# Performance work log

Hardware: AMD Instinct MI355X
Metric: run time of the kernel (lower is better)

The kernel has to match this reference:

```python
import jax, jax.numpy as jnp
import numpy as np

PC_RANGE = (-54.0, -54.0, -5.0, 54.0, 54.0, 3.0)
VOXEL = (0.075, 0.075, 0.2)
STRIDE = 8
FW = 180  # feature map size along x
FH = 180  # feature map size along y
NUM_CLASS = 2
M = 500   # num_max_objs
MIN_RADIUS = 2
OVERLAP = 0.1
C_IN = 128
HM_C = 2
REG_C = 9
B = 4


def conv2d(x, w, b=None):
    y = jax.lax.conv_general_dilated(x, w, (1, 1), 'SAME',
                                     dimension_numbers=('NCHW', 'OIHW', 'NCHW'))
    return y if b is None else y + b[None, :, None, None]


def bn(x, g, b, m, v, eps=1e-5):
    inv = g / jnp.sqrt(v + eps)
    return x * inv[None, :, None, None] + (b - m * inv)[None, :, None, None]


def gaussian_radius(height, width, min_overlap):
    # centernet_utils.gaussian_radius
    b1 = height + width
    c1 = width * height * (1.0 - min_overlap) / (1.0 + min_overlap)
    r1 = (b1 + jnp.sqrt(jnp.maximum(b1 * b1 - 4.0 * c1, 0.0))) / 2.0
    b2 = 2.0 * (height + width)
    c2 = (1.0 - min_overlap) * width * height
    r2 = (b2 + jnp.sqrt(jnp.maximum(b2 * b2 - 16.0 * c2, 0.0))) / 2.0
    a3 = 4.0 * min_overlap
    b3 = -2.0 * min_overlap * (height + width)
    c3 = (min_overlap - 1.0) * width * height
    r3 = (b3 + jnp.sqrt(jnp.maximum(b3 * b3 - 4.0 * a3 * c3, 0.0))) / (2.0 * a3)
    return jnp.minimum(jnp.minimum(r1, r2), r3)


def assign_targets(gt):
    # gt: (B, M, 8) = [x, y, z, dx, dy, dz, ry, cls]; cls==0 / zero box = padding
    x, y, z = gt[..., 0], gt[..., 1], gt[..., 2]
    dx, dy, dz, ry = gt[..., 3], gt[..., 4], gt[..., 5], gt[..., 6]
    cls = gt[..., 7].astype(jnp.int32)
    coord_x = jnp.clip((x - PC_RANGE[0]) / VOXEL[0] / STRIDE, 0.0, FW - 0.5)
    coord_y = jnp.clip((y - PC_RANGE[1]) / VOXEL[1] / STRIDE, 0.0, FH - 0.5)
    cxi = coord_x.astype(jnp.int32)
    cyi = coord_y.astype(jnp.int32)
    dxp = dx / VOXEL[0] / STRIDE
    dyp = dy / VOXEL[1] / STRIDE
    radius = jnp.maximum(gaussian_radius(dxp, dyp, OVERLAP).astype(jnp.int32), MIN_RADIUS)
    valid = (dxp > 0) & (dyp > 0)
    pos = valid & (cls >= 1)

    # --- dense gaussian splat, max-reduced per class (= draw_gaussian_to_heatmap) ---
    ddx = jnp.arange(FW)[None, None, :] - cxi[..., None]   # (B,M,FW)
    ddy = jnp.arange(FH)[None, None, :] - cyi[..., None]   # (B,M,FH)
    sigma = (2.0 * radius.astype(jnp.float32) + 1.0) / 6.0
    d2 = (ddy[..., :, None] ** 2 + ddx[..., None, :] ** 2).astype(jnp.float32)  # (B,M,FH,FW)
    g = jnp.exp(-d2 / (2.0 * sigma[..., None, None] ** 2))
    win = (jnp.abs(ddy) <= radius[..., None])[..., :, None] & \
          (jnp.abs(ddx) <= radius[..., None])[..., None, :]
    g = jnp.where(win & pos[..., None, None], g, 0.0)
    seg = jnp.where(pos, cls - 1, NUM_CLASS)
    hmv = jax.vmap(lambda gv, sv: jax.ops.segment_max(gv, sv, num_segments=NUM_CLASS + 1))(
        g.reshape(B, M, FH * FW), seg)
    heatmap = jnp.maximum(hmv[:, :NUM_CLASS].reshape(B, NUM_CLASS, FH, FW), 0.0)
    heatmap_mask = (heatmap > 0).astype(gt.dtype)

    # --- inds / mask / ret_boxes (5 slots per object: center + 4 neighbors) ---
    base_ind = cyi * FW + cxi
    w_cond = VOXEL[0] * STRIDE > dy / 4.0   # faithful: uses temp_w = gt[:,4]
    l_cond = VOXEL[1] * STRIDE > dx / 4.0   # faithful: uses temp_l = gt[:,3]
    left = cxi - 1 >= 0
    right = cxi + 1 < FW
    up = cyi - 1 >= 0
    down = cyi + 1 < FH
    m0 = jnp.where(valid, jnp.where(cls >= 1, 1, -1), 0)
    s1 = valid & ~w_cond & left
    s2 = valid & ~w_cond & right
    s3 = valid & ~l_cond & up
    s4 = valid & ~l_cond & down
    mask = jnp.stack([m0,
                      jnp.where(s1, m0, 0), jnp.where(s2, m0, 0),
                      jnp.where(s3, m0, 0), jnp.where(s4, m0, 0)], -1).reshape(B, 5 * M)
    inds = jnp.stack([jnp.where(valid, base_ind, 0),
                      jnp.where(s1, base_ind - 1, 0), jnp.where(s2, base_ind + 1, 0),
                      jnp.where(s3, base_ind - FW, 0), jnp.where(s4, base_ind + FW, 0)],
                     -1).reshape(B, 5 * M).astype(jnp.int32)
    offx = coord_x - cxi.astype(gt.dtype)
    offy = coord_y - cyi.astype(gt.dtype)
    base = jnp.stack([offx, offy, z,
                      jnp.log(jnp.maximum(dx, 1e-8)),
                      jnp.log(jnp.maximum(dy, 1e-8)),
                      jnp.log(jnp.maximum(dz, 1e-8)),
                      jnp.cos(ry), jnp.sin(ry)], -1)          # (B,M,8)
    z5 = jnp.zeros((B, M), gt.dtype)
    dx_adj = jnp.stack([z5, s1.astype(gt.dtype), -s2.astype(gt.dtype), z5, z5], -1)  # (B,M,5)
    dy_adj = jnp.stack([z5, z5, z5, s3.astype(gt.dtype), -s4.astype(gt.dtype)], -1)
    zero5 = jnp.zeros_like(dx_adj)
    delta = jnp.stack([dx_adj, dy_adj, zero5, zero5, zero5, zero5, zero5, zero5], -1)  # (B,M,5,8)
    rb = (base[:, :, None, :] + delta) * valid[:, :, None, None].astype(gt.dtype)
    ret_boxes = rb.reshape(B, 5 * M, 8)
    return heatmap, ret_boxes, inds, mask, heatmap_mask


def setup_inputs():
    key = jax.random.key(0)
    ks = jax.random.split(key, 12)
    x = jax.random.normal(ks[0], (B, C_IN, FH, FW), jnp.float32)
    # realistic gt boxes; last 150 per scene are zero padding
    cxy = jax.random.uniform(ks[1], (B, M, 2), minval=-50.0, maxval=50.0)
    zc = jax.random.uniform(ks[2], (B, M, 1), minval=-2.0, maxval=1.0)
    dims = jax.random.uniform(ks[3], (B, M, 3), minval=0.5, maxval=6.0)
    ry = jax.random.uniform(ks[4], (B, M, 1), minval=-3.14, maxval=3.14)
    cls = jax.random.randint(ks[5], (B, M, 1), 1, NUM_CLASS + 1).astype(jnp.float32)
    vm = (jnp.arange(M) < 350)[None, :, None].astype(jnp.float32)
    gt_boxes = jnp.concatenate([cxy, zc, dims, ry, cls], -1) * vm
    p = lambda k, s, sc: jax.random.normal(k, s, jnp.float32) * sc
    return {
        'x': x, 'gt_boxes': gt_boxes,
        'conv1_w': p(ks[6], (C_IN, C_IN, 3, 3), 0.02),
        'bn1_g': jnp.ones((C_IN,)), 'bn1_b': jnp.zeros((C_IN,)),
        'bn1_m': jnp.zeros((C_IN,)), 'bn1_v': jnp.ones((C_IN,)),
        'conv2_w': p(ks[7], (C_IN, C_IN, 3, 3), 0.02),
        'bn2_g': jnp.ones((C_IN,)), 'bn2_b': jnp.zeros((C_IN,)),
        'bn2_m': jnp.zeros((C_IN,)), 'bn2_v': jnp.ones((C_IN,)),
        'hm_w': p(ks[8], (HM_C, C_IN, 3, 3), 0.02),
        'hm_b': jnp.full((HM_C,), -2.19, jnp.float32),
        'reg_w': p(ks[9], (REG_C, C_IN, 3, 3), 0.001),
        'reg_b': jnp.zeros((REG_C,), jnp.float32),
    }


def reference(x, gt_boxes, conv1_w, bn1_g, bn1_b, bn1_m, bn1_v,
              conv2_w, bn2_g, bn2_b, bn2_m, bn2_v, hm_w, hm_b, reg_w, reg_b):
    f = jax.nn.relu(bn(conv2d(x, conv1_w), bn1_g, bn1_b, bn1_m, bn1_v))
    f = jax.nn.relu(bn(conv2d(f, conv2_w), bn2_g, bn2_b, bn2_m, bn2_v))
    hm = conv2d(f, hm_w, hm_b)      # (B, 2, H, W)
    reg = conv2d(f, reg_w, reg_b)   # (B, 9, H, W)
    heatmap, ret_boxes, inds, mask, heatmap_mask = assign_targets(gt_boxes)
    return hm, reg, heatmap, ret_boxes, inds, mask, heatmap_mask
```

## Files before the change

### kernel.cpp

```cpp
#include <hip/hip_runtime.h>
#include <math.h>

typedef unsigned short u16;
typedef short bf16x8 __attribute__((ext_vector_type(8)));
typedef float f32x4 __attribute__((ext_vector_type(4)));

#define FW_ 180
#define FH_ 180
#define HW_ (FW_*FH_)
#define CIN_ 128
#define BB_ 4
#define MM_ 500
#define PW_ 182
#define PADE ((size_t)BB_*PW_*PW_*CIN_)

#define HM_OFF   0
#define REG_OFF  (BB_*2*HW_)
#define HEAT_OFF (REG_OFF + BB_*9*HW_)
#define RB_OFF   (HEAT_OFF + BB_*2*HW_)
#define IND_OFF  (RB_OFF + BB_*MM_*5*8)
#define MSK_OFF  (IND_OFF + BB_*MM_*5)
#define HMM_OFF  (MSK_OFF + BB_*MM_*5)

__device__ inline u16 f2bf(float f) {
    unsigned u = __float_as_uint(f);
    u += 0x7FFFu + ((u >> 16) & 1u);
    return (u16)(u >> 16);
}

#define GLOAD_LDS16(gsrc, ldst) \
    __builtin_amdgcn_global_load_lds( \
        (const __attribute__((address_space(1))) unsigned*)(gsrc), \
        (__attribute__((address_space(3))) unsigned*)(ldst), 16, 0, 0)

__global__ void k_init(u16* __restrict__ ws, float* __restrict__ out)
{
    int idx = blockIdx.x * 256 + threadIdx.x;
    const int n1 = 3 * BB_ * PW_ * PW_;
    if (idx < n1) {
        int buf = idx / (BB_ * PW_ * PW_);
        int rem = idx % (BB_ * PW_ * PW_);
        int p = rem % (PW_ * PW_);
        int r = p / PW_, c = p % PW_;
        if (r > 0 && r < PW_ - 1 && c > 0 && c < PW_ - 1) return;
        u16* base = ws + (size_t)buf * PADE + (size_t)rem * CIN_;
#pragma unroll
        for (int i = 0; i < 16; ++i) ((uint4*)base)[i] = make_uint4(0, 0, 0, 0);
    } else {
        int i = idx - n1;
        if (i < BB_ * 2 * HW_) out[HEAT_OFF + i] = 0.f;
    }
}

__global__ __launch_bounds__(256) void k_prep_xT(const float* __restrict__ in,
                                                 u16* __restrict__ xT)
{
    __shared__ unsigned lt32[180 * 65];
    int tid = threadIdx.x;
    int row = blockIdx.x, b = blockIdx.y;
    const float* inr = in + ((size_t)b * CIN_ * FH_ + row) * FW_;
    for (int i = tid; i < 64 * 45; i += 256) {
        int ci2 = i / 45, c4 = i - 45 * ci2;
        const float* p0 = inr + (size_t)(2 * ci2) * HW_ + c4 * 4;
        float4 a = *(const float4*)p0;
        float4 bq = *(const float4*)(p0 + HW_);
        lt32[(c4 * 4 + 0) * 65 + ci2] = (unsigned)f2bf(a.x) | ((unsigned)f2bf(bq.x) << 16);
        lt32[(c4 * 4 + 1) * 65 + ci2] = (unsigned)f2bf(a.y) | ((unsigned)f2bf(bq.y) << 16);
        lt32[(c4 * 4 + 2) * 65 + ci2] = (unsigned)f2bf(a.z) | ((unsigned)f2bf(bq.z) << 16);
        lt32[(c4 * 4 + 3) * 65 + ci2] = (unsigned)f2bf(a.w) | ((unsigned)f2bf(bq.w) << 16);
    }
    __syncthreads();
    unsigned* dst = (unsigned*)(xT + ((size_t)b * PW_ * PW_ + (size_t)(row + 1) * PW_ + 1) * CIN_);
    for (int idx = tid; idx < 180 * 64; idx += 256) {
        int col = idx >> 6, c2 = idx & 63;
        dst[col * 64 + c2] = lt32[col * 65 + c2];
    }
}

__global__ void k_prep_w(const float* __restrict__ w1, const float* __restrict__ w2,
                         const float* __restrict__ hw, const float* __restrict__ rw,
                         u16* __restrict__ wT1, u16* __restrict__ wT2,
                         u16* __restrict__ wTh)
{
    int i = blockIdx.x * 256 + threadIdx.x;
    const int NW = 9 * CIN_ * CIN_;
    if (i < NW) {
        int tap = i / (CIN_ * CIN_);
        int r = i % (CIN_ * CIN_);
        int co = r >> 7, ci = r & 127;
        wT1[i] = f2bf(w1[((size_t)co * CIN_ + ci) * 9 + tap]);
    } else if (i < 2 * NW) {
        int j = i - NW;
        int tap = j / (CIN_ * CIN_);
        int r = j % (CIN_ * CIN_);
        int co = r >> 7, ci = r & 127;
        wT2[j] = f2bf(w2[((size_t)co * CIN_ + ci) * 9 + tap]);
    } else {
        int j = i - 2 * NW;
        if (j >= 9 * 16 * CIN_) return;
        int tap = j / (16 * CIN_);
        int r = j % (16 * CIN_);
        int co = r >> 7, ci = r & 127;
        float v = 0.f;
        if (co < 2)       v = hw[((size_t)co * CIN_ + ci) * 9 + tap];
        else if (co < 11) v = rw[((size_t)(co - 2) * CIN_ + ci) * 9 + tap];
        wTh[j] = f2bf(v);
    }
}

__global__ __launch_bounds__(256) void k_conv_v5(
    const u16* __restrict__ xT, const u16* __restrict__ wT,
    const float* __restrict__ gg, const float* __restrict__ bbn,
    const float* __restrict__ mmn, const float* __restrict__ vvn,
    u16* __restrict__ yT)
{
    __shared__ u16 lin[1600 * 8];
    __shared__ u16 lwt[2304 * 8];

    int tid  = threadIdx.x;
    int wv   = tid >> 6, lane = tid & 63;
    int lm   = lane & 15, hi = lane >> 4;
    int csp  = blockIdx.x % 3, cog = blockIdx.x / 3;
    int C0   = (csp == 2) ? 116 : csp * 64;
    int cob  = cog * 64;
    int R0   = blockIdx.y * 4;
    int b    = blockIdx.z;
    const u16* xb = xT + (size_t)b * PW_ * PW_ * CIN_;

    f32x4 acc[4][4];
#pragma unroll
    for (int i = 0; i < 4; ++i)
#pragma unroll
        for (int j = 0; j < 4; ++j) acc[i][j] = (f32x4){0.f, 0.f, 0.f, 0.f};

    const int wco = (tid & 255) >> 2;
    const int wq  = (tid & 3) ^ ((wco >> 1) & 3);

#pragma unroll 1
    for (int ch = 0; ch < 4; ++ch) {
        int ci0 = ch * 32;
        __syncthreads();
#pragma unroll
        for (int rd = 0; rd < 6; ++rd) {
            int o = rd * 256 + tid;
            int rc = o >> 2;
            int r = rc / 66, c = rc - 66 * r;
            int q = (o & 3) ^ ((c >> 1) & 3);
            const u16* src = xb + ((size_t)(R0 + r) * PW_ + (C0 + c)) * CIN_ + ci0 + q * 8;
            GLOAD_LDS16(src, &lin[(size_t)(rd * 256 + wv * 64) * 8]);
        }
        if (wv == 0) {
            int o = 1536 + lane;
            int rc = o >> 2;
            int r = rc / 66, c = rc - 66 * r;
            if (o >= 1584) { r = 5; c = 65; }
            int q = (o & 3) ^ ((c >> 1) & 3);
            const u16* src = xb + ((size_t)(R0 + r) * PW_ + (C0 + c)) * CIN_ + ci0 + q * 8;
            GLOAD_LDS16(src, &lin[(size_t)1536 * 8]);
        }
#pragma unroll
        for (int tap = 0; tap < 9; ++tap) {
            const u16* src = wT + (size_t)tap * CIN_ * CIN_ + (size_t)(cob + wco) * CIN_ + ci0 + wq * 8;
            GLOAD_LDS16(src, &lwt[(size_t)(tap * 256 + wv * 64) * 8]);
        }
        __syncthreads();

#pragma unroll
        for (int tap = 0; tap < 9; ++tap) {
            const int kr = tap / 3, kc = tap - 3 * (tap / 3);
            bf16x8 av[4];
#pragma unroll
            for (int mf = 0; mf < 4; ++mf) {
                int col = mf * 16 + lm;
                int unit = tap * 256 + col * 4 + (hi ^ ((col >> 1) & 3));
                av[mf] = *(const bf16x8*)&lwt[(size_t)unit * 8];
            }
#pragma unroll
            for (int nf = 0; nf < 4; ++nf) {
                int c = wv * 16 + lm + kc;
                int rc = (nf + kr) * 66 + c;
                int unit = rc * 4 + (hi ^ ((c >> 1) & 3));
                bf16x8 bv = *(const bf16x8*)&lin[(size_t)unit * 8];
#pragma unroll
                for (int mf = 0; mf < 4; ++mf)
                    acc[mf][nf] = __builtin_amdgcn_mfma_f32_16x16x32_bf16(
                        av[mf], bv, acc[mf][nf], 0, 0, 0);
            }
        }
    }

#pragma unroll
    for (int mf = 0; mf < 4; ++mf) {
        int co0 = cob + mf * 16 + hi * 4;
        float4 g4 = *(const float4*)(gg + co0);
        float4 b4 = *(const float4*)(bbn + co0);
        float4 m4 = *(const float4*)(mmn + co0);
        float4 v4 = *(const float4*)(vvn + co0);
        float sc0 = g4.x / sqrtf(v4.x + 1e-5f), sh0 = b4.x - m4.x * sc0;
        float sc1 = g4.y / sqrtf(v4.y + 1e-5f), sh1 = b4.y - m4.y * sc1;
        float sc2 = g4.z / sqrtf(v4.z + 1e-5f), sh2 = b4.z - m4.z * sc2;
        float sc3 = g4.w / sqrtf(v4.w + 1e-5f), sh3 = b4.w - m4.w * sc3;
#pragma unroll
        for (int nf = 0; nf < 4; ++nf) {
            f32x4 A = acc[mf][nf];
            float y0 = fmaxf(fmaf(A[0], sc0, sh0), 0.f);
            float y1 = fmaxf(fmaf(A[1], sc1, sh1), 0.f);
            float y2 = fmaxf(fmaf(A[2], sc2, sh2), 0.f);
            float y3 = fmaxf(fmaf(A[3], sc3, sh3), 0.f);
            unsigned p0 = (unsigned)f2bf(y0) | ((unsigned)f2bf(y1) << 16);
            unsigned p1 = (unsigned)f2bf(y2) | ((unsigned)f2bf(y3) << 16);
            u16* op = yT + (size_t)b * PW_ * PW_ * CIN_ +
                      ((size_t)(R0 + nf + 1) * PW_ + (C0 + wv * 16 + lm + 1)) * CIN_ + co0;
            *(uint2*)op = make_uint2(p0, p1);
        }
    }
}

__global__ __launch_bounds__(256) void k_head_v5(
    const u16* __restrict__ f2T, const u16* __restrict__ wTh,
    const float* __restrict__ hb, const float* __restrict__ rb,
    float* __restrict__ out)
{
    __shared__ u16 lin[1600 * 8];
    __shared__ u16 lwt[2304 * 8];

    int tid  = threadIdx.x;
    int wv   = tid >> 6, lane = tid & 63;
    int lm   = lane & 15, hi = lane >> 4;
    int csp  = blockIdx.x;
    int C0   = (csp == 2) ? 116 : csp * 64;
    int R0   = blockIdx.y * 4;
    int b    = blockIdx.z;
    const u16* xb = f2T + (size_t)b * PW_ * PW_ * CIN_;

    f32x4 acc[4];
#pragma unroll
    for (int i = 0; i < 4; ++i) acc[i] = (f32x4){0.f, 0.f, 0.f, 0.f};

#pragma unroll
    for (int rd = 0; rd < 9; ++rd) {
        int o = rd * 256 + tid;
        int tap = o >> 8, rest = o & 255;
        int co = rest >> 4, u8s = rest & 15;
        const u16* src = wTh + (size_t)tap * 16 * CIN_ + co * CIN_ + ((u8s ^ (co & 7)) * 8);
        GLOAD_LDS16(src, &lwt[(size_t)(rd * 256 + wv * 64) * 8]);
    }

#pragma unroll 1
    for (int ch = 0; ch < 4; ++ch) {
        int ci0 = ch * 32;
        __syncthreads();
#pragma unroll
        for (int rd = 0; rd < 6; ++rd) {
            int o = rd * 256 + tid;
            int rc = o >> 2;
            int r = rc / 66, c = rc - 66 * r;
            int q = (o & 3) ^ ((c >> 1) & 3);
            const u16* src = xb + ((size_t)(R0 + r) * PW_ + (C0 + c)) * CIN_ + ci0 + q * 8;
            GLOAD_LDS16(src, &lin[(size_t)(rd * 256 + wv * 64) * 8]);
        }
        if (wv == 0) {
            int o = 1536 + lane;
            int rc = o >> 2;
            int r = rc / 66, c = rc - 66 * r;
            if (o >= 1584) { r = 5; c = 65; }
            int q = (o & 3) ^ ((c >> 1) & 3);
            const u16* src = xb + ((size_t)(R0 + r) * PW_ + (C0 + c)) * CIN_ + ci0 + q * 8;
            GLOAD_LDS16(src, &lin[(size_t)1536 * 8]);
        }
        __syncthreads();

#pragma unroll
        for (int tap = 0; tap < 9; ++tap) {
            const int kr = tap / 3, kc = tap - 3 * (tap / 3);
            int u8 = (ch * 4 + hi) ^ (lm & 7);
            bf16x8 av = *(const bf16x8*)&lwt[(size_t)(tap * 256 + lm * 16 + u8) * 8];
#pragma unroll
            for (int nf = 0; nf < 4; ++nf) {
                int c = wv * 16 + lm + kc;
                int rc = (nf + kr) * 66 + c;
                int unit = rc * 4 + (hi ^ ((c >> 1) & 3));
                bf16x8 bv = *(const bf16x8*)&lin[(size_t)unit * 8];
                acc[nf] = __builtin_amdgcn_mfma_f32_16x16x32_bf16(av, bv, acc[nf], 0, 0, 0);
            }
        }
    }

#pragma unroll
    for (int nf = 0; nf < 4; ++nf) {
        int row = R0 + nf, col = C0 + wv * 16 + lm;
        f32x4 A = acc[nf];
#pragma unroll
        for (int r = 0; r < 4; ++r) {
            int co = hi * 4 + r;
            float v = A[r];
            if (co < 2)
                out[HM_OFF + ((size_t)(b * 2 + co)) * HW_ + (size_t)row * FW_ + col] = v + hb[co];
            else if (co < 11)
                out[REG_OFF + ((size_t)(b * 9 + co - 2)) * HW_ + (size_t)row * FW_ + col] = v + rb[co - 2];
        }
    }
}

__global__ void k_objects(const float* __restrict__ gt, float* __restrict__ out)
{
    int ob = blockIdx.x;
    int b = ob / MM_, m = ob % MM_;
    const float* gp = gt + (size_t)ob * 8;
    float x = gp[0], y = gp[1], z = gp[2];
    float dx = gp[3], dy = gp[4], dz = gp[5], ry = gp[6];
    int cls = (int)gp[7];

    float coord_x = fminf(fmaxf((x + 54.f) / 0.075f / 8.f, 0.f), 179.5f);
    float coord_y = fminf(fmaxf((y + 54.f) / 0.075f / 8.f, 0.f), 179.5f);
    int cxi = (int)coord_x, cyi = (int)coord_y;
    float dxp = dx / 0.075f / 8.f;
    float dyp = dy / 0.075f / 8.f;

    float hgt = dxp, wid = dyp, mo = 0.1f;
    float b1 = hgt + wid, c1 = wid * hgt * (1.f - mo) / (1.f + mo);
    float r1 = (b1 + sqrtf(fmaxf(b1 * b1 - 4.f * c1, 0.f))) * 0.5f;
    float b2 = 2.f * (hgt + wid), c2 = (1.f - mo) * wid * hgt;
    float r2 = (b2 + sqrtf(fmaxf(b2 * b2 - 16.f * c2, 0.f))) * 0.5f;
    float a3 = 4.f * mo, b3 = -2.f * mo * (hgt + wid), c3 = (mo - 1.f) * wid * hgt;
    float r3 = (b3 + sqrtf(fmaxf(b3 * b3 - 4.f * a3 * c3, 0.f))) / (2.f * a3);
    int radius = max((int)fminf(fminf(r1, r2), r3), 2);

    bool valid = (dxp > 0.f) && (dyp > 0.f);
    bool pos = valid && (cls >= 1);

    if (threadIdx.x == 0) {
        float m0 = valid ? (cls >= 1 ? 1.f : -1.f) : 0.f;
        bool w_cond = (0.075f * 8.f) > dy / 4.f;
        bool l_cond = (0.075f * 8.f) > dx / 4.f;
        bool s1 = valid && !w_cond && (cxi - 1 >= 0);
        bool s2 = valid && !w_cond && (cxi + 1 < FW_);
        bool s3 = valid && !l_cond && (cyi - 1 >= 0);
        bool s4 = valid && !l_cond && (cyi + 1 < FH_);
        int base_ind = cyi * FW_ + cxi;

        float* indp = out + IND_OFF + (size_t)b * MM_ * 5 + m * 5;
        float* mskp = out + MSK_OFF + (size_t)b * MM_ * 5 + m * 5;
        indp[0] = valid ? (float)base_ind : 0.f;
        indp[1] = s1 ? (float)(base_ind - 1) : 0.f;
        indp[2] = s2 ? (float)(base_ind + 1) : 0.f;
        indp[3] = s3 ? (float)(base_ind - FW_) : 0.f;
        indp[4] = s4 ? (float)(base_ind + FW_) : 0.f;
        mskp[0] = m0;
        mskp[1] = s1 ? m0 : 0.f;
        mskp[2] = s2 ? m0 : 0.f;
        mskp[3] = s3 ? m0 : 0.f;
        mskp[4] = s4 ? m0 : 0.f;

        float offx = coord_x - (float)cxi;
        float offy = coord_y - (float)cyi;
        float bse[8] = { offx, offy, z,
                         logf(fmaxf(dx, 1e-8f)), logf(fmaxf(dy, 1e-8f)),
                         logf(fmaxf(dz, 1e-8f)), cosf(ry), sinf(ry) };
        float vm = valid ? 1.f : 0.f;
        float* rbp = out + RB_OFF + ((size_t)b * MM_ + m) * 5 * 8;
#pragma unroll
        for (int s = 0; s < 5; ++s) {
            float t0 = bse[0], t1 = bse[1];
            if (s == 1) t0 += s1 ? 1.f : 0.f;
            if (s == 2) t0 -= s2 ? 1.f : 0.f;
            if (s == 3) t1 += s3 ? 1.f : 0.f;
            if (s == 4) t1 -= s4 ? 1.f : 0.f;
            rbp[s * 8 + 0] = t0 * vm;
            rbp[s * 8 + 1] = t1 * vm;
#pragma unroll
            for (int k = 2; k < 8; ++k) rbp[s * 8 + k] = bse[k] * vm;
        }
    }

    if (pos) {
        float sigma = (2.f * (float)radius + 1.f) / 6.f;
        float inv2s2 = 1.f / (2.f * sigma * sigma);
        int x0 = max(cxi - radius, 0), x1 = min(cxi + radius, FW_ - 1);
        int y0 = max(cyi - radius, 0), y1 = min(cyi + radius, FH_ - 1);
        int wdt = x1 - x0 + 1, tot = wdt * (y1 - y0 + 1);
        float* hp = out + HEAT_OFF + (size_t)(b * 2 + (cls - 1)) * HW_;
        for (int i = threadIdx.x; i < tot; i += blockDim.x) {
            int yy = y0 + i / wdt, xx = x0 + i % wdt;
            float ddy = (float)(yy - cyi), ddx = (float)(xx - cxi);
            float gvl = expf(-(ddy * ddy + ddx * ddx) * inv2s2);
            atomicMax((int*)(hp + yy * FW_ + xx), __float_as_int(gvl));
        }
    }
}

__global__ void k_hm_mask(float* __restrict__ out)
{
    int i = blockIdx.x * 256 + threadIdx.x;
    if (i < BB_ * 2 * HW_) {
        float v = out[HEAT_OFF + i];
        out[HMM_OFF + i] = v > 0.f ? 1.f : 0.f;
    }
}

extern "C" void kernel_launch(void* const* d_in, const int* in_sizes, int n_in,
                              void* d_out, int out_size, void* d_ws, size_t ws_size,
                              hipStream_t stream)
{
    const float* x  = (const float*)d_in[0];
    const float* gt = (const float*)d_in[1];
    const float* w1 = (const float*)d_in[2];
    const float* g1 = (const float*)d_in[3];
    const float* b1 = (const float*)d_in[4];
    const float* m1 = (const float*)d_in[5];
    const float* v1 = (const float*)d_in[6];
    const float* w2 = (const float*)d_in[7];
    const float* g2 = (const float*)d_in[8];
    const float* b2 = (const float*)d_in[9];
    const float* m2 = (const float*)d_in[10];
    const float* v2 = (const float*)d_in[11];
    const float* hw = (const float*)d_in[12];
    const float* hb = (const float*)d_in[13];
    const float* rw = (const float*)d_in[14];
    const float* rb = (const float*)d_in[15];
    float* out = (float*)d_out;

    u16* ws  = (u16*)d_ws;
    u16* xT  = ws;
    u16* f1T = ws + PADE;
    u16* f2T = ws + 2 * PADE;
    u16* wT1 = ws + 3 * PADE;
    u16* wT2 = wT1 + 9 * CIN_ * CIN_;
    u16* wTh = wT2 + 9 * CIN_ * CIN_;

    const int NINIT = 3 * BB_ * PW_ * PW_ + BB_ * 2 * HW_;
    k_init<<<(NINIT + 255) / 256, 256, 0, stream>>>(ws, out);
    k_prep_xT<<<dim3(180, BB_), 256, 0, stream>>>(x, xT);
    const int NWALL = 2 * 9 * CIN_ * CIN_ + 9 * 16 * CIN_;
    k_prep_w<<<(NWALL + 255) / 256, 256, 0, stream>>>(w1, w2, hw, rw, wT1, wT2, wTh);

    dim3 cg(6, 45, BB_);
    k_conv_v5<<<cg, 256, 0, stream>>>(xT,  wT1, g1, b1, m1, v1, f1T);
    k_conv_v5<<<cg, 256, 0, stream>>>(f1T, wT2, g2, b2, m2, v2, f2T);

    dim3 hg(3, 45, BB_);
    k_head_v5<<<hg, 256, 0, stream>>>(f2T, wTh, hb, rb, out);

    k_objects<<<BB_ * MM_, 64, 0, stream>>>(gt, out);
    k_hm_mask<<<(BB_ * 2 * HW_ + 255) / 256, 256, 0, stream>>>(out);
}
```

Baseline: 158.3 us.

## Double-buffer conv input tiles, read weights from global, merge output-channel blocks

```diff
diff --git a/kernel.cpp b/kernel.cpp
--- a/kernel.cpp
+++ b/kernel.cpp
@@ -71,9 +71,14 @@
     }
     __syncthreads();
     unsigned* dst = (unsigned*)(xT + ((size_t)b * PW_ * PW_ + (size_t)(row + 1) * PW_ + 1) * CIN_);
-    for (int idx = tid; idx < 180 * 64; idx += 256) {
-        int col = idx >> 6, c2 = idx & 63;
-        dst[col * 64 + c2] = lt32[col * 65 + c2];
+    for (int idx = tid; idx < 180 * 16; idx += 256) {
+        int col = idx >> 4, q = idx & 15;
+        uint4 v;
+        v.x = lt32[col * 65 + q * 4 + 0];
+        v.y = lt32[col * 65 + q * 4 + 1];
+        v.z = lt32[col * 65 + q * 4 + 2];
+        v.w = lt32[col * 65 + q * 4 + 3];
+        *(uint4*)&dst[col * 64 + q * 4] = v;
     }
 }
 
@@ -108,21 +113,20 @@
     }
 }
 
-__global__ __launch_bounds__(256) void k_conv_v5(
+__global__ __launch_bounds__(512, 3) void k_conv_v6(
     const u16* __restrict__ xT, const u16* __restrict__ wT,
     const float* __restrict__ gg, const float* __restrict__ bbn,
     const float* __restrict__ mmn, const float* __restrict__ vvn,
     u16* __restrict__ yT)
 {
-    __shared__ u16 lin[1600 * 8];
-    __shared__ u16 lwt[2304 * 8];
+    __shared__ u16 lin[2][1600 * 8];
 
     int tid  = threadIdx.x;
     int wv   = tid >> 6, lane = tid & 63;
     int lm   = lane & 15, hi = lane >> 4;
-    int csp  = blockIdx.x % 3, cog = blockIdx.x / 3;
+    int wm   = wv >> 2, wn = wv & 3;
+    int csp  = blockIdx.x;
     int C0   = (csp == 2) ? 116 : csp * 64;
-    int cob  = cog * 64;
     int R0   = blockIdx.y * 4;
     int b    = blockIdx.z;
     const u16* xb = xT + (size_t)b * PW_ * PW_ * CIN_;
@@ -133,65 +137,69 @@
 #pragma unroll
         for (int j = 0; j < 4; ++j) acc[i][j] = (f32x4){0.f, 0.f, 0.f, 0.f};
 
-    const int wco = (tid & 255) >> 2;
-    const int wq  = (tid & 3) ^ ((wco >> 1) & 3);
-
-#pragma unroll 1
+    size_t soff[3];
+#pragma unroll
+    for (int rd = 0; rd < 3; ++rd) {
+        int o = rd * 512 + tid;
+        int rc = o >> 2;
+        int r = rc / 66, c = rc - 66 * r;
+        int q = (o & 3) ^ ((c >> 1) & 3);
+        soff[rd] = ((size_t)(R0 + r) * PW_ + (C0 + c)) * CIN_ + q * 8;
+    }
+    size_t soffX = 0;
+    if (tid < 64) {
+        int o = 1536 + tid;
+        int rc = o >> 2;
+        int r = rc / 66, c = rc - 66 * r;
+        if (o >= 1584) { r = 5; c = 65; }
+        int q = (o & 3) ^ ((c >> 1) & 3);
+        soffX = ((size_t)(R0 + r) * PW_ + (C0 + c)) * CIN_ + q * 8;
+    }
+
+    const u16* aB = wT + ((size_t)(wm * 64 + lm)) * CIN_ + hi * 8;
+
+#pragma unroll
+    for (int rd = 0; rd < 3; ++rd)
+        GLOAD_LDS16(xb + soff[rd], &lin[0][(size_t)(rd * 512 + wv * 64) * 8]);
+    if (tid < 64) GLOAD_LDS16(xb + soffX, &lin[0][(size_t)1536 * 8]);
+    __syncthreads();
+
+#pragma unroll
     for (int ch = 0; ch < 4; ++ch) {
-        int ci0 = ch * 32;
-        __syncthreads();
-#pragma unroll
-        for (int rd = 0; rd < 6; ++rd) {
-            int o = rd * 256 + tid;
-            int rc = o >> 2;
-            int r = rc / 66, c = rc - 66 * r;
-            int q = (o & 3) ^ ((c >> 1) & 3);
-            const u16* src = xb + ((size_t)(R0 + r) * PW_ + (C0 + c)) * CIN_ + ci0 + q * 8;
-            GLOAD_LDS16(src, &lin[(size_t)(rd * 256 + wv * 64) * 8]);
-        }
-        if (wv == 0) {
-            int o = 1536 + lane;
-            int rc = o >> 2;
-            int r = rc / 66, c = rc - 66 * r;
-            if (o >= 1584) { r = 5; c = 65; }
-            int q = (o & 3) ^ ((c >> 1) & 3);
-            const u16* src = xb + ((size_t)(R0 + r) * PW_ + (C0 + c)) * CIN_ + ci0 + q * 8;
-            GLOAD_LDS16(src, &lin[(size_t)1536 * 8]);
-        }
-#pragma unroll
-        for (int tap = 0; tap < 9; ++tap) {
-            const u16* src = wT + (size_t)tap * CIN_ * CIN_ + (size_t)(cob + wco) * CIN_ + ci0 + wq * 8;
-            GLOAD_LDS16(src, &lwt[(size_t)(tap * 256 + wv * 64) * 8]);
-        }
-        __syncthreads();
-
+        const int ci0 = ch * 32;
+        const int cur = ch & 1;
 #pragma unroll
         for (int tap = 0; tap < 9; ++tap) {
             const int kr = tap / 3, kc = tap - 3 * (tap / 3);
             bf16x8 av[4];
 #pragma unroll
-            for (int mf = 0; mf < 4; ++mf) {
-                int col = mf * 16 + lm;
-                int unit = tap * 256 + col * 4 + (hi ^ ((col >> 1) & 3));
-                av[mf] = *(const bf16x8*)&lwt[(size_t)unit * 8];
-            }
+            for (int mf = 0; mf < 4; ++mf)
+                av[mf] = *(const bf16x8*)(aB + (size_t)tap * CIN_ * CIN_ + mf * 16 * CIN_ + ci0);
 #pragma unroll
             for (int nf = 0; nf < 4; ++nf) {
-                int c = wv * 16 + lm + kc;
+                int c = wn * 16 + lm + kc;
                 int rc = (nf + kr) * 66 + c;
                 int unit = rc * 4 + (hi ^ ((c >> 1) & 3));
-                bf16x8 bv = *(const bf16x8*)&lin[(size_t)unit * 8];
+                bf16x8 bv = *(const bf16x8*)&lin[cur][(size_t)unit * 8];
 #pragma unroll
                 for (int mf = 0; mf < 4; ++mf)
                     acc[mf][nf] = __builtin_amdgcn_mfma_f32_16x16x32_bf16(
                         av[mf], bv, acc[mf][nf], 0, 0, 0);
             }
         }
+        if (ch < 3) {
+            const int ci1 = ci0 + 32;
+#pragma unroll
+            for (int rd = 0; rd < 3; ++rd)
+                GLOAD_LDS16(xb + soff[rd] + ci1, &lin[cur ^ 1][(size_t)(rd * 512 + wv * 64) * 8]);
+            if (tid < 64) GLOAD_LDS16(xb + soffX + ci1, &lin[cur ^ 1][(size_t)1536 * 8]);
+        }
+        __syncthreads();
     }
 
 #pragma unroll
     for (int mf = 0; mf < 4; ++mf) {
-        int co0 = cob + mf * 16 + hi * 4;
+        int co0 = wm * 64 + mf * 16 + hi * 4;
         float4 g4 = *(const float4*)(gg + co0);
         float4 b4 = *(const float4*)(bbn + co0);
         float4 m4 = *(const float4*)(mmn + co0);
@@ -210,19 +218,18 @@
             unsigned p0 = (unsigned)f2bf(y0) | ((unsigned)f2bf(y1) << 16);
             unsigned p1 = (unsigned)f2bf(y2) | ((unsigned)f2bf(y3) << 16);
             u16* op = yT + (size_t)b * PW_ * PW_ * CIN_ +
-                      ((size_t)(R0 + nf + 1) * PW_ + (C0 + wv * 16 + lm + 1)) * CIN_ + co0;
+                      ((size_t)(R0 + nf + 1) * PW_ + (C0 + wn * 16 + lm + 1)) * CIN_ + co0;
             *(uint2*)op = make_uint2(p0, p1);
         }
     }
 }
 
-__global__ __launch_bounds__(256) void k_head_v5(
+__global__ __launch_bounds__(256, 3) void k_head_v6(
     const u16* __restrict__ f2T, const u16* __restrict__ wTh,
     const float* __restrict__ hb, const float* __restrict__ rb,
     float* __restrict__ out)
 {
-    __shared__ u16 lin[1600 * 8];
-    __shared__ u16 lwt[2304 * 8];
+    __shared__ u16 lin[2][1600 * 8];
 
     int tid  = threadIdx.x;
     int wv   = tid >> 6, lane = tid & 63;
@@ -237,53 +244,58 @@
 #pragma unroll
     for (int i = 0; i < 4; ++i) acc[i] = (f32x4){0.f, 0.f, 0.f, 0.f};
 
-#pragma unroll
-    for (int rd = 0; rd < 9; ++rd) {
+    size_t soff[6];
+#pragma unroll
+    for (int rd = 0; rd < 6; ++rd) {
         int o = rd * 256 + tid;
-        int tap = o >> 8, rest = o & 255;
-        int co = rest >> 4, u8s = rest & 15;
-        const u16* src = wTh + (size_t)tap * 16 * CIN_ + co * CIN_ + ((u8s ^ (co & 7)) * 8);
-        GLOAD_LDS16(src, &lwt[(size_t)(rd * 256 + wv * 64) * 8]);
-    }
-
-#pragma unroll 1
+        int rc = o >> 2;
+        int r = rc / 66, c = rc - 66 * r;
+        int q = (o & 3) ^ ((c >> 1) & 3);
+        soff[rd] = ((size_t)(R0 + r) * PW_ + (C0 + c)) * CIN_ + q * 8;
+    }
+    size_t soffX = 0;
+    if (tid < 64) {
+        int o = 1536 + tid;
+        int rc = o >> 2;
+        int r = rc / 66, c = rc - 66 * r;
+        if (o >= 1584) { r = 5; c = 65; }
+        int q = (o & 3) ^ ((c >> 1) & 3);
+        soffX = ((size_t)(R0 + r) * PW_ + (C0 + c)) * CIN_ + q * 8;
+    }
+
+    const u16* aB = wTh + (size_t)lm * CIN_ + hi * 8;
+
+#pragma unroll
+    for (int rd = 0; rd < 6; ++rd)
+        GLOAD_LDS16(xb + soff[rd], &lin[0][(size_t)(rd * 256 + wv * 64) * 8]);
+    if (tid < 64) GLOAD_LDS16(xb + soffX, &lin[0][(size_t)1536 * 8]);
+    __syncthreads();
+
+#pragma unroll
     for (int ch = 0; ch < 4; ++ch) {
-        int ci0 = ch * 32;
-        __syncthreads();
-#pragma unroll
-        for (int rd = 0; rd < 6; ++rd) {
-            int o = rd * 256 + tid;
-            int rc = o >> 2;
-            int r = rc / 66, c = rc - 66 * r;
-            int q = (o & 3) ^ ((c >> 1) & 3);
-            const u16* src = xb + ((size_t)(R0 + r) * PW_ + (C0 + c)) * CIN_ + ci0 + q * 8;
-            GLOAD_LDS16(src, &lin[(size_t)(rd * 256 + wv * 64) * 8]);
-        }
-        if (wv == 0) {
-            int o = 1536 + lane;
-            int rc = o >> 2;
-            int r = rc / 66, c = rc - 66 * r;
-            if (o >= 1584) { r = 5; c = 65; }
-            int q = (o & 3) ^ ((c >> 1) & 3);
-            const u16* src = xb + ((size_t)(R0 + r) * PW_ + (C0 + c)) * CIN_ + ci0 + q * 8;
-            GLOAD_LDS16(src, &lin[(size_t)1536 * 8]);
-        }
-        __syncthreads();
-
+        const int ci0 = ch * 32;
+        const int cur = ch & 1;
 #pragma unroll
         for (int tap = 0; tap < 9; ++tap) {
             const int kr = tap / 3, kc = tap - 3 * (tap / 3);
-            int u8 = (ch * 4 + hi) ^ (lm & 7);
-            bf16x8 av = *(const bf16x8*)&lwt[(size_t)(tap * 256 + lm * 16 + u8) * 8];
+            bf16x8 av = *(const bf16x8*)(aB + (size_t)tap * 16 * CIN_ + ci0);
 #pragma unroll
             for (int nf = 0; nf < 4; ++nf) {
                 int c = wv * 16 + lm + kc;
                 int rc = (nf + kr) * 66 + c;
                 int unit = rc * 4 + (hi ^ ((c >> 1) & 3));
-                bf16x8 bv = *(const bf16x8*)&lin[(size_t)unit * 8];
+                bf16x8 bv = *(const bf16x8*)&lin[cur][(size_t)unit * 8];
                 acc[nf] = __builtin_amdgcn_mfma_f32_16x16x32_bf16(av, bv, acc[nf], 0, 0, 0);
             }
         }
+        if (ch < 3) {
+            const int ci1 = ci0 + 32;
+#pragma unroll
+            for (int rd = 0; rd < 6; ++rd)
+                GLOAD_LDS16(xb + soff[rd] + ci1, &lin[cur ^ 1][(size_t)(rd * 256 + wv * 64) * 8]);
+            if (tid < 64) GLOAD_LDS16(xb + soffX + ci1, &lin[cur ^ 1][(size_t)1536 * 8]);
+        }
+        __syncthreads();
     }
 
 #pragma unroll
@@ -434,12 +446,12 @@
     const int NWALL = 2 * 9 * CIN_ * CIN_ + 9 * 16 * CIN_;
     k_prep_w<<<(NWALL + 255) / 256, 256, 0, stream>>>(w1, w2, hw, rw, wT1, wT2, wTh);
 
-    dim3 cg(6, 45, BB_);
-    k_conv_v5<<<cg, 256, 0, stream>>>(xT,  wT1, g1, b1, m1, v1, f1T);
-    k_conv_v5<<<cg, 256, 0, stream>>>(f1T, wT2, g2, b2, m2, v2, f2T);
+    dim3 cg(3, 45, BB_);
+    k_conv_v6<<<cg, 512, 0, stream>>>(xT,  wT1, g1, b1, m1, v1, f1T);
+    k_conv_v6<<<cg, 512, 0, stream>>>(f1T, wT2, g2, b2, m2, v2, f2T);
 
     dim3 hg(3, 45, BB_);
-    k_head_v5<<<hg, 256, 0, stream>>>(f2T, wTh, hb, rb, out);
+    k_head_v6<<<hg, 256, 0, stream>>>(f2T, wTh, hb, rb, out);
 
     k_objects<<<BB_ * MM_, 64, 0, stream>>>(gt, out);
     k_hm_mask<<<(BB_ * 2 * HW_ + 255) / 256, 256, 0, stream>>>(out);
```

After: 359.6 us. 2.27x slower.

## Double conv row tile to 8 rows with 512-thread blocks sharing weight tiles

Applied to the files above, without the earlier changes.

```diff
diff --git a/kernel.cpp b/kernel.cpp
--- a/kernel.cpp
+++ b/kernel.cpp
@@ -71,9 +71,14 @@
     }
     __syncthreads();
     unsigned* dst = (unsigned*)(xT + ((size_t)b * PW_ * PW_ + (size_t)(row + 1) * PW_ + 1) * CIN_);
-    for (int idx = tid; idx < 180 * 64; idx += 256) {
-        int col = idx >> 6, c2 = idx & 63;
-        dst[col * 64 + c2] = lt32[col * 65 + c2];
+    for (int idx = tid; idx < 180 * 16; idx += 256) {
+        int col = idx >> 4, q = idx & 15;
+        uint4 v;
+        v.x = lt32[col * 65 + q * 4 + 0];
+        v.y = lt32[col * 65 + q * 4 + 1];
+        v.z = lt32[col * 65 + q * 4 + 2];
+        v.w = lt32[col * 65 + q * 4 + 3];
+        *(uint4*)&dst[col * 64 + q * 4] = v;
     }
 }
 
@@ -108,22 +113,24 @@
     }
 }
 
-__global__ __launch_bounds__(256) void k_conv_v5(
+__global__ __launch_bounds__(512, 4) void k_conv_v8(
     const u16* __restrict__ xT, const u16* __restrict__ wT,
     const float* __restrict__ gg, const float* __restrict__ bbn,
     const float* __restrict__ mmn, const float* __restrict__ vvn,
     u16* __restrict__ yT)
 {
-    __shared__ u16 lin[1600 * 8];
+    __shared__ u16 lin[2640 * 8];
     __shared__ u16 lwt[2304 * 8];
 
     int tid  = threadIdx.x;
     int wv   = tid >> 6, lane = tid & 63;
     int lm   = lane & 15, hi = lane >> 4;
+    int wg   = wv >> 2, wn = wv & 3;
     int csp  = blockIdx.x % 3, cog = blockIdx.x / 3;
     int C0   = (csp == 2) ? 116 : csp * 64;
     int cob  = cog * 64;
-    int R0   = blockIdx.y * 4;
+    int rt   = blockIdx.y;
+    int R0   = (rt == 22) ? 172 : rt * 8;
     int b    = blockIdx.z;
     const u16* xb = xT + (size_t)b * PW_ * PW_ * CIN_;
 
@@ -133,36 +140,55 @@
 #pragma unroll
         for (int j = 0; j < 4; ++j) acc[i][j] = (f32x4){0.f, 0.f, 0.f, 0.f};
 
-    const int wco = (tid & 255) >> 2;
-    const int wq  = (tid & 3) ^ ((wco >> 1) & 3);
-
-#pragma unroll 1
+    unsigned soffI[5];
+#pragma unroll
+    for (int rd = 0; rd < 5; ++rd) {
+        int o = rd * 512 + tid;
+        int rc = o >> 2;
+        int r = rc / 66, c = rc - 66 * r;
+        int q = (o & 3) ^ ((c >> 1) & 3);
+        soffI[rd] = (unsigned)(((R0 + r) * PW_ + (C0 + c)) * CIN_ + q * 8);
+    }
+    unsigned soffIX = 0;
+    if (tid < 80) {
+        int o = 2560 + tid;
+        int rc = o >> 2;
+        int r = rc / 66, c = rc - 66 * r;
+        int q = (o & 3) ^ ((c >> 1) & 3);
+        soffIX = (unsigned)(((R0 + r) * PW_ + (C0 + c)) * CIN_ + q * 8);
+    }
+    unsigned soffW[4];
+#pragma unroll
+    for (int rd = 0; rd < 4; ++rd) {
+        int u = rd * 512 + tid;
+        int tap = u >> 8, rest = u & 255;
+        int col = rest >> 2;
+        int q = (rest & 3) ^ ((col >> 1) & 3);
+        soffW[rd] = (unsigned)(tap * CIN_ * CIN_ + (cob + col) * CIN_ + q * 8);
+    }
+    unsigned soffWX = 0;
+    if (tid < 256) {
+        int u = 2048 + tid;
+        int tap = u >> 8, rest = u & 255;
+        int col = rest >> 2;
+        int q = (rest & 3) ^ ((col >> 1) & 3);
+        soffWX = (unsigned)(tap * CIN_ * CIN_ + (cob + col) * CIN_ + q * 8);
+    }
+
+#pragma unroll
     for (int ch = 0; ch < 4; ++ch) {
-        int ci0 = ch * 32;
+        const int ci0 = ch * 32;
         __syncthreads();
 #pragma unroll
-        for (int rd = 0; rd < 6; ++rd) {
-            int o = rd * 256 + tid;
-            int rc = o >> 2;
-            int r = rc / 66, c = rc - 66 * r;
-            int q = (o & 3) ^ ((c >> 1) & 3);
-            const u16* src = xb + ((size_t)(R0 + r) * PW_ + (C0 + c)) * CIN_ + ci0 + q * 8;
-            GLOAD_LDS16(src, &lin[(size_t)(rd * 256 + wv * 64) * 8]);
-        }
-        if (wv == 0) {
-            int o = 1536 + lane;
-            int rc = o >> 2;
-            int r = rc / 66, c = rc - 66 * r;
-            if (o >= 1584) { r = 5; c = 65; }
-            int q = (o & 3) ^ ((c >> 1) & 3);
-            const u16* src = xb + ((size_t)(R0 + r) * PW_ + (C0 + c)) * CIN_ + ci0 + q * 8;
-            GLOAD_LDS16(src, &lin[(size_t)1536 * 8]);
-        }
-#pragma unroll
-        for (int tap = 0; tap < 9; ++tap) {
-            const u16* src = wT + (size_t)tap * CIN_ * CIN_ + (size_t)(cob + wco) * CIN_ + ci0 + wq * 8;
-            GLOAD_LDS16(src, &lwt[(size_t)(tap * 256 + wv * 64) * 8]);
-        }
+        for (int rd = 0; rd < 5; ++rd)
+            GLOAD_LDS16(xb + soffI[rd] + ci0, &lin[(size_t)(rd * 512 + wv * 64) * 8]);
+        if (tid < 80)
+            GLOAD_LDS16(xb + soffIX + ci0, &lin[(size_t)(2560 + wv * 64) * 8]);
+#pragma unroll
+        for (int rd = 0; rd < 4; ++rd)
+            GLOAD_LDS16(wT + soffW[rd] + ci0, &lwt[(size_t)(rd * 512 + wv * 64) * 8]);
+        if (tid < 256)
+            GLOAD_LDS16(wT + soffWX + ci0, &lwt[(size_t)(2048 + wv * 64) * 8]);
         __syncthreads();
 
 #pragma unroll
@@ -177,8 +203,8 @@
             }
 #pragma unroll
             for (int nf = 0; nf < 4; ++nf) {
-                int c = wv * 16 + lm + kc;
-                int rc = (nf + kr) * 66 + c;
+                int c = wn * 16 + lm + kc;
+                int rc = (wg * 4 + nf + kr) * 66 + c;
                 int unit = rc * 4 + (hi ^ ((c >> 1) & 3));
                 bf16x8 bv = *(const bf16x8*)&lin[(size_t)unit * 8];
 #pragma unroll
@@ -210,7 +236,7 @@
             unsigned p0 = (unsigned)f2bf(y0) | ((unsigned)f2bf(y1) << 16);
             unsigned p1 = (unsigned)f2bf(y2) | ((unsigned)f2bf(y3) << 16);
             u16* op = yT + (size_t)b * PW_ * PW_ * CIN_ +
-                      ((size_t)(R0 + nf + 1) * PW_ + (C0 + wv * 16 + lm + 1)) * CIN_ + co0;
+                      ((size_t)(R0 + wg * 4 + nf + 1) * PW_ + (C0 + wn * 16 + lm + 1)) * CIN_ + co0;
             *(uint2*)op = make_uint2(p0, p1);
         }
     }
@@ -259,8 +285,8 @@
             const u16* src = xb + ((size_t)(R0 + r) * PW_ + (C0 + c)) * CIN_ + ci0 + q * 8;
             GLOAD_LDS16(src, &lin[(size_t)(rd * 256 + wv * 64) * 8]);
         }
-        if (wv == 0) {
-            int o = 1536 + lane;
+        if (tid < 64) {
+            int o = 1536 + tid;
             int rc = o >> 2;
             int r = rc / 66, c = rc - 66 * r;
             if (o >= 1584) { r = 5; c = 65; }
@@ -434,9 +460,9 @@
     const int NWALL = 2 * 9 * CIN_ * CIN_ + 9 * 16 * CIN_;
     k_prep_w<<<(NWALL + 255) / 256, 256, 0, stream>>>(w1, w2, hw, rw, wT1, wT2, wTh);
 
-    dim3 cg(6, 45, BB_);
-    k_conv_v5<<<cg, 256, 0, stream>>>(xT,  wT1, g1, b1, m1, v1, f1T);
-    k_conv_v5<<<cg, 256, 0, stream>>>(f1T, wT2, g2, b2, m2, v2, f2T);
+    dim3 cg(6, 23, BB_);
+    k_conv_v8<<<cg, 512, 0, stream>>>(xT,  wT1, g1, b1, m1, v1, f1T);
+    k_conv_v8<<<cg, 512, 0, stream>>>(f1T, wT2, g2, b2, m2, v2, f2T);
 
     dim3 hg(3, 45, BB_);
     k_head_v5<<<hg, 256, 0, stream>>>(f2T, wTh, hb, rb, out);
```

Measured after the change: 279.4 us. +76.5%, slower.
